# Kernel optimization log

Hardware: AMD Instinct MI355X
Metric: run time of the kernel (lower is better)

The kernel has to match this reference:

```python
import jax, jax.numpy as jnp
import numpy as np

N_NODES = 50000
N_EDGES = 800000
N_GRAPHS = 256
NEG_SLOPE = 0.2

def selu(x):
    return jax.nn.selu(x)

def gat_conv(x, src, dst, W, att_l, att_r, b, n_nodes):
    """PyG GATConv, heads=1, with self-loops already appended to (src, dst).
    Message j->i: alpha_ij = softmax_i(leaky_relu(a_l.h_j + a_r.h_i)); out_i = sum_j alpha_ij h_j + b."""
    h = x @ W                                   # [N, C]
    a_src = h @ att_l                           # [N]
    a_dst = h @ att_r                           # [N]
    e = jax.nn.leaky_relu(a_src[src] + a_dst[dst], NEG_SLOPE)   # [E]
    # segment softmax over incoming edges of each dst node
    m = jax.ops.segment_max(e, dst, num_segments=n_nodes)       # [N]
    m = jnp.where(jnp.isfinite(m), m, 0.0)
    ex = jnp.exp(e - m[dst])
    denom = jax.ops.segment_sum(ex, dst, num_segments=n_nodes)  # [N]
    alpha = ex / jnp.maximum(denom, 1e-16)[dst]                  # [E]
    out = jax.ops.segment_sum(h[src] * alpha[:, None], dst, num_segments=n_nodes)
    return out + b

def global_mean_pool(x, batch, n_graphs):
    s = jax.ops.segment_sum(x, batch, num_segments=n_graphs)
    cnt = jax.ops.segment_sum(jnp.ones((x.shape[0],), x.dtype), batch, num_segments=n_graphs)
    return s / jnp.maximum(cnt, 1.0)[:, None]

def setup_inputs() -> dict:
    key = jax.random.key(0)
    ks = jax.random.split(key, 12)
    F_in, C, H, NC = 310, 256, 128, 2
    x = jax.random.normal(ks[0], (N_NODES, F_in), dtype=jnp.float32)
    edge_index = jax.random.randint(ks[1], (2, N_EDGES), 0, N_NODES, dtype=jnp.int64)
    batch = jnp.sort(jax.random.randint(ks[2], (N_NODES,), 0, N_GRAPHS, dtype=jnp.int64))
    g = lambda k, shp: jax.random.normal(k, shp, dtype=jnp.float32) * 0.05
    return {
        "x": x, "edge_index": edge_index, "batch": batch,
        "W1": g(ks[3], (F_in, C)), "att_l1": g(ks[4], (C,)), "att_r1": g(ks[5], (C,)),
        "b1": jnp.zeros((C,), jnp.float32),
        "W2": g(ks[6], (C, C)), "att_l2": g(ks[7], (C,)), "att_r2": g(ks[8], (C,)),
        "b2": jnp.zeros((C,), jnp.float32),
        "fc1_W": g(ks[9], (C, H)), "fc1_b": jnp.zeros((H,), jnp.float32),
        "fc2_W": g(ks[10], (H, NC)), "fc2_b": jnp.zeros((NC,), jnp.float32),
    }

def reference(x, edge_index, batch, W1, att_l1, att_r1, b1, W2, att_l2, att_r2, b2,
              fc1_W, fc1_b, fc2_W, fc2_b):
    n = x.shape[0]
    loops = jnp.arange(n, dtype=edge_index.dtype)
    src = jnp.concatenate([edge_index[0], loops])   # add_self_loops=True (PyG default)
    dst = jnp.concatenate([edge_index[1], loops])
    h = selu(gat_conv(x, src, dst, W1, att_l1, att_r1, b1, n))
    h = selu(gat_conv(h, src, dst, W2, att_l2, att_r2, b2, n))
    g = selu(global_mean_pool(h, batch, N_GRAPHS))      # [G, 256]
    g = selu(g @ fc1_W + fc1_b)                         # [G, 128]
    # dropout is identity in eval mode
    return jax.nn.log_softmax(g @ fc2_W + fc2_b, axis=-1)  # [G, 2]
```

## Files before the change

### kernel.cpp

```cpp
#include <hip/hip_runtime.h>
#include <hip/hip_bf16.h>

#define N_NODES 50000
#define N_EDGES 800000
#define N_TOT   (N_EDGES + N_NODES)
#define N_GRAPHS 256
#define F_IN 310
#define KP1 320
#define CH 256
#define HID 128
#define CST 264

typedef __attribute__((ext_vector_type(8))) short short8;
typedef __attribute__((ext_vector_type(4))) float f32x4;
typedef unsigned short ushort_t;

__device__ __forceinline__ float selu_f(float x) {
    const float scale = 1.0507009873554805f;
    const float alpha = 1.6732632423543772f;
    return x > 0.f ? scale * x : scale * alpha * (expm1f(x));
}

__device__ __forceinline__ ushort_t f32_to_bf16_rne(float f) {
    unsigned u = __float_as_uint(f);
    unsigned rounding = 0x7FFFu + ((u >> 16) & 1u);
    return (ushort_t)((u + rounding) >> 16);
}
__device__ __forceinline__ float bf16_to_f32(ushort_t v) {
    return __uint_as_float(((unsigned)v) << 16);
}

#define WT_BLKS ((CH * KP1 + CH * CH + 255) / 256)
__global__ __launch_bounds__(256) void convert_wt_deg(
        const float* __restrict__ W1, ushort_t* __restrict__ W1t,
        const float* __restrict__ W2, ushort_t* __restrict__ W2t,
        const int* __restrict__ ei, int* __restrict__ deg) {
    int b = blockIdx.x;
    if (b < WT_BLKS) {
        int i = b * 256 + threadIdx.x;
        const int n1 = CH * KP1;
        if (i < n1) {
            int n = i / KP1, k = i % KP1;
            W1t[i] = (k < F_IN) ? f32_to_bf16_rne(W1[(long)k * CH + n]) : 0;
        } else {
            int j = i - n1;
            if (j >= CH * CH) return;
            int n = j / CH, k = j % CH;
            W2t[j] = f32_to_bf16_rne(W2[(long)k * CH + n]);
        }
    } else {
        int eid = (b - WT_BLKS) * 256 + threadIdx.x;
        if (eid >= N_TOT) return;
        int d = (eid < N_EDGES) ? ei[N_EDGES + eid] : eid - N_EDGES;
        atomicAdd(&deg[d], 1);
    }
}

template<int AF32, int FILL>
__global__ __launch_bounds__(256, 4) void gemm_k(
        const void* __restrict__ Asrc, const ushort_t* __restrict__ Bt,
        ushort_t* __restrict__ Cb, const float* __restrict__ att_l,
        const float* __restrict__ att_r, float* __restrict__ a_srcv,
        float* __restrict__ a_dstv, int M, int Kp, int gemmBlocks,
        const int* __restrict__ ei, int* __restrict__ fillpos,
        const int* __restrict__ startA, ushort_t* __restrict__ csr_src) {
    __shared__ __align__(16) ushort_t smem[20480];
    ushort_t (*As)[2048] = reinterpret_cast<ushort_t(*)[2048]>(smem);
    ushort_t (*Bs)[8192] = reinterpret_cast<ushort_t(*)[8192]>(smem + 4096);
    int tid = threadIdx.x;

    if constexpr (FILL) {
        if ((int)blockIdx.x >= gemmBlocks) {
            int eid = ((int)blockIdx.x - gemmBlocks) * 256 + tid;
            if (eid < N_TOT) {
                if (eid < N_EDGES) {
                    int s = ei[eid], d = ei[N_EDGES + eid];
                    int p = atomicAdd(&fillpos[d], 1);
                    csr_src[p] = (ushort_t)s;
                } else {
                    int d = eid - N_EDGES;
                    csr_src[startA[d]] = (ushort_t)d;
                }
            }
            return;
        }
    }

    int row0 = blockIdx.x * 64;
    int w = tid >> 6, l = tid & 63;
    int lr = l & 15, lc = l >> 4;
    f32x4 acc[4][4] = {};

    int srow = l >> 2;
    int sc = l & 3;
    int sx = sc ^ (srow & 3) ^ ((srow >> 2) & 3);
    int garow = row0 + w * 16 + srow; if (garow >= M) garow = M - 1;
    const ushort_t* gB[4];
#pragma unroll
    for (int g = 0; g < 4; ++g)
        gB[g] = Bt + (size_t)(w * 64 + g * 16 + srow) * Kp + sx * 8;
    int nt = Kp >> 5;

    const ushort_t* gA = nullptr;
    const float* xrow = nullptr;
    if (AF32) xrow = (const float*)Asrc + (size_t)garow * F_IN;
    else      gA = (const ushort_t*)Asrc + (size_t)garow * Kp + sx * 8;

    auto stageB = [&](int sel, int k0) {
#pragma unroll
        for (int g = 0; g < 4; ++g)
            __builtin_amdgcn_global_load_lds(
                (const __attribute__((address_space(1))) void*)(gB[g] + k0),
                (__attribute__((address_space(3))) void*)(&Bs[sel][(w * 64 + g * 16) * 32]), 16, 0, 0);
    };
    auto stageA_glds = [&](int sel, int k0) {
        __builtin_amdgcn_global_load_lds(
            (const __attribute__((address_space(1))) void*)(gA + k0),
            (__attribute__((address_space(3))) void*)(&As[sel][w * 16 * 32]), 16, 0, 0);
    };
    float va[8];
    auto loadA_f32 = [&](int k0) {
        int kc = k0 + sc * 8;
        if (kc + 8 <= F_IN) {
#pragma unroll
            for (int j = 0; j < 4; ++j) {
                float2 p = *(const float2*)(xrow + kc + j * 2);
                va[j * 2] = p.x; va[j * 2 + 1] = p.y;
            }
        } else {
#pragma unroll
            for (int j = 0; j < 8; ++j)
                va[j] = (kc + j < F_IN) ? xrow[kc + j] : 0.f;
        }
    };
    auto writeA = [&](int sel) {
        short8 s;
#pragma unroll
        for (int j = 0; j < 8; ++j) s[j] = (short)f32_to_bf16_rne(va[j]);
        *(short8*)(&As[sel][(w * 16 + srow) * 32 + sx * 8]) = s;
    };

    if (AF32) loadA_f32(0); else stageA_glds(0, 0);
    stageB(0, 0);
    if (AF32) writeA(0);
    __syncthreads();
    int cur = 0;
    for (int t = 0; t < nt; ++t) {
        int k1 = (t + 1) << 5;
        if (t + 1 < nt) {
            if (AF32) loadA_f32(k1); else stageA_glds(cur ^ 1, k1);
            stageB(cur ^ 1, k1);
        }
        short8 af[4], bfv[4];
#pragma unroll
        for (int mi = 0; mi < 4; ++mi) {
            int r = mi * 16 + lr;
            af[mi] = *(const short8*)(&As[cur][r * 32 + ((lc ^ (r & 3) ^ ((r >> 2) & 3)) * 8)]);
        }
#pragma unroll
        for (int ni = 0; ni < 4; ++ni) {
            int r = w * 64 + ni * 16 + lr;
            bfv[ni] = *(const short8*)(&Bs[cur][r * 32 + ((lc ^ (r & 3) ^ ((r >> 2) & 3)) * 8)]);
        }
#pragma unroll
        for (int mi = 0; mi < 4; ++mi)
#pragma unroll
            for (int ni = 0; ni < 4; ++ni)
                acc[mi][ni] = __builtin_amdgcn_mfma_f32_16x16x32_bf16(
                    bfv[ni], af[mi], acc[mi][ni], 0, 0, 0);
        if (AF32 && t + 1 < nt) writeA(cur ^ 1);
        __syncthreads();
        cur ^= 1;
    }

    ushort_t* Ct  = smem;
    float*    s_pw = (float*)(smem + 17024);
    float pl[4] = {}, pr[4] = {};
#pragma unroll
    for (int ni = 0; ni < 4; ++ni) {
        float4 alv = *(const float4*)(att_l + w * 64 + ni * 16 + lc * 4);
        float4 arv = *(const float4*)(att_r + w * 64 + ni * 16 + lc * 4);
#pragma unroll
        for (int mi = 0; mi < 4; ++mi) {
            f32x4 v = acc[mi][ni];
            pl[mi] += v[0] * alv.x + v[1] * alv.y + v[2] * alv.z + v[3] * alv.w;
            pr[mi] += v[0] * arv.x + v[1] * arv.y + v[2] * arv.z + v[3] * arv.w;
            ushort4 cv;
            cv.x = f32_to_bf16_rne(v[0]); cv.y = f32_to_bf16_rne(v[1]);
            cv.z = f32_to_bf16_rne(v[2]); cv.w = f32_to_bf16_rne(v[3]);
            *(ushort4*)(Ct + (mi * 16 + lr) * CST + w * 64 + ni * 16 + lc * 4) = cv;
        }
    }
#pragma unroll
    for (int mi = 0; mi < 4; ++mi) {
        pl[mi] += __shfl_xor(pl[mi], 16); pl[mi] += __shfl_xor(pl[mi], 32);
        pr[mi] += __shfl_xor(pr[mi], 16); pr[mi] += __shfl_xor(pr[mi], 32);
    }
    if (l < 16) {
#pragma unroll
        for (int mi = 0; mi < 4; ++mi) {
            s_pw[w * 64 + mi * 16 + lr]       = pl[mi];
            s_pw[256 + w * 64 + mi * 16 + lr] = pr[mi];
        }
    }
    __syncthreads();
#pragma unroll
    for (int it = 0; it < 8; ++it) {
        int id = it * 256 + tid;
        int r = id >> 5, c8 = (id & 31) * 8;
        int grow = row0 + r;
        if (grow < M) {
            short8 v = *(const short8*)(Ct + r * CST + c8);
            *(short8*)(Cb + (size_t)grow * CH + c8) = v;
        }
    }
    if (tid < 64) {
        int grow = row0 + tid;
        if (grow < M) {
            a_srcv[grow] = s_pw[tid] + s_pw[64 + tid] + s_pw[128 + tid] + s_pw[192 + tid];
            a_dstv[grow] = s_pw[256 + tid] + s_pw[320 + tid] + s_pw[384 + tid] + s_pw[448 + tid];
        }
    }
}

__global__ __launch_bounds__(256) void reserve_k(
        const int* __restrict__ deg, int* __restrict__ start,
        int* __restrict__ fillpos, int* __restrict__ cursor, int n) {
    int i = blockIdx.x * blockDim.x + threadIdx.x;
    if (i >= n) return;
    int s = atomicAdd(cursor, deg[i]);
    start[i] = s;
    fillpos[i] = s + 1;
}

__global__ __launch_bounds__(256) void gat_aggregate(
        const int* __restrict__ start, const int* __restrict__ deg,
        const ushort_t* __restrict__ csr_src,
        const float* __restrict__ a_src, const float* __restrict__ a_dst,
        const ushort_t* __restrict__ h, const float* __restrict__ bias,
        ushort_t* __restrict__ out_bf, int n) {
    int wid = threadIdx.x >> 6;
    int lane = threadIdx.x & 63;
    int node = blockIdx.x * 4 + wid;
    if (node >= n) return;
    int s0 = start[node];
    int dg = deg[node];
    float ad = a_dst[node];

    float sum_l = 0.f;
    float4 acc = {0.f, 0.f, 0.f, 0.f};
    for (int c = 0; c < dg; c += 64) {
        int nc = min(64, dg - c);
        int s_l = 0; float ex_l = 0.f;
        if (lane < nc) {
            s_l = csr_src[s0 + c + lane];
            float e = a_src[s_l] + ad;
            e = fmaxf(e, 0.2f * e);
            ex_l = __expf(e);
            sum_l += ex_l;
        }
        int j = 0;
        for (; j + 8 <= nc; j += 8) {
            int si[8]; float xi[8]; ushort4 hv[8];
#pragma unroll
            for (int k = 0; k < 8; ++k) {
                si[k] = __shfl(s_l, j + k);
                xi[k] = __shfl(ex_l, j + k);
            }
#pragma unroll
            for (int k = 0; k < 8; ++k)
                hv[k] = *(const ushort4*)(h + (long)si[k] * CH + lane * 4);
#pragma unroll
            for (int k = 0; k < 8; ++k) {
                acc.x += xi[k] * bf16_to_f32(hv[k].x);
                acc.y += xi[k] * bf16_to_f32(hv[k].y);
                acc.z += xi[k] * bf16_to_f32(hv[k].z);
                acc.w += xi[k] * bf16_to_f32(hv[k].w);
            }
        }
        for (; j < nc; ++j) {
            int sj = __shfl(s_l, j);
            float xj = __shfl(ex_l, j);
            ushort4 hv = *(const ushort4*)(h + (long)sj * CH + lane * 4);
            acc.x += xj * bf16_to_f32(hv.x);
            acc.y += xj * bf16_to_f32(hv.y);
            acc.z += xj * bf16_to_f32(hv.z);
            acc.w += xj * bf16_to_f32(hv.w);
        }
    }
    float sum = sum_l;
#pragma unroll
    for (int off = 32; off > 0; off >>= 1) sum += __shfl_xor(sum, off);
    float inv = 1.f / fmaxf(sum, 1e-16f);

    float4 bv = *(const float4*)(bias + lane * 4);
    ushort4 ob;
    ob.x = f32_to_bf16_rne(selu_f(acc.x * inv + bv.x));
    ob.y = f32_to_bf16_rne(selu_f(acc.y * inv + bv.y));
    ob.z = f32_to_bf16_rne(selu_f(acc.z * inv + bv.z));
    ob.w = f32_to_bf16_rne(selu_f(acc.w * inv + bv.w));
    *(ushort4*)(out_bf + (long)node * CH + lane * 4) = ob;
}

__global__ __launch_bounds__(1024) void pool_head_kernel(
        const ushort_t* __restrict__ h, const int* __restrict__ batch,
        const float* __restrict__ fc1W, const float* __restrict__ fc1b,
        const float* __restrict__ fc2W, const float* __restrict__ fc2b,
        float* __restrict__ out) {
    __shared__ float part[4][CH];
    __shared__ float row[CH];
    __shared__ float part2[8][HID];
    __shared__ float hrow[HID];
    __shared__ float logits[2];
    int g = blockIdx.x;
    int tid = threadIdx.x;
    int t = tid & 255;
    int quad = tid >> 8;
    int lo, hi;
    { int a = 0, b = N_NODES;
      while (a < b) { int mid = (a + b) >> 1; if (batch[mid] < g) a = mid + 1; else b = mid; }
      lo = a; }
    { int a = lo, b = N_NODES;
      while (a < b) { int mid = (a + b) >> 1; if (batch[mid] < g + 1) a = mid + 1; else b = mid; }
      hi = a; }
    float a0 = 0.f, a1 = 0.f;
    int i = lo + quad;
    for (; i + 4 < hi; i += 8) {
        a0 += bf16_to_f32(h[(long)i * CH + t]);
        a1 += bf16_to_f32(h[(long)(i + 4) * CH + t]);
    }
    for (; i < hi; i += 4) a0 += bf16_to_f32(h[(long)i * CH + t]);
    part[quad][t] = a0 + a1;
    __syncthreads();
    if (quad == 0) {
        float cnt = (float)(hi - lo);
        float acc = (part[0][t] + part[1][t]) + (part[2][t] + part[3][t]);
        row[t] = selu_f(acc / fmaxf(cnt, 1.f));
    }
    __syncthreads();
    {
        int o = tid & 127;
        int seg = tid >> 7;
        float s = 0.f;
        int k0 = seg * 32;
        for (int k = k0; k < k0 + 32; ++k) s += row[k] * fc1W[k * HID + o];
        part2[seg][o] = s;
    }
    __syncthreads();
    if (tid < HID) {
        float s = fc1b[tid];
#pragma unroll
        for (int j = 0; j < 8; ++j) s += part2[j][tid];
        hrow[tid] = selu_f(s);
    }
    __syncthreads();
    if (tid < 2) {
        float a = fc2b[tid];
        for (int k = 0; k < HID; k++) a += hrow[k] * fc2W[k * 2 + tid];
        logits[tid] = a;
    }
    __syncthreads();
    if (tid < 2) {
        float m = fmaxf(logits[0], logits[1]);
        float lse = logf(expf(logits[0] - m) + expf(logits[1] - m)) + m;
        out[g * 2 + tid] = logits[tid] - lse;
    }
}

extern "C" void kernel_launch(void* const* d_in, const int* in_sizes, int n_in,
                              void* d_out, int out_size, void* d_ws, size_t ws_size,
                              hipStream_t stream) {
    const float* x      = (const float*)d_in[0];
    const int*   ei     = (const int*)d_in[1];
    const int*   batch  = (const int*)d_in[2];
    const float* W1     = (const float*)d_in[3];
    const float* att_l1 = (const float*)d_in[4];
    const float* att_r1 = (const float*)d_in[5];
    const float* b1     = (const float*)d_in[6];
    const float* W2     = (const float*)d_in[7];
    const float* att_l2 = (const float*)d_in[8];
    const float* att_r2 = (const float*)d_in[9];
    const float* b2     = (const float*)d_in[10];
    const float* fc1W   = (const float*)d_in[11];
    const float* fc1b   = (const float*)d_in[12];
    const float* fc2W   = (const float*)d_in[13];
    const float* fc2b   = (const float*)d_in[14];
    float* out = (float*)d_out;

    char* ws = (char*)d_ws;
    size_t off = 0;
    auto alloc = [&](size_t bytes) {
        void* p = ws + off;
        off += (bytes + 255) & ~(size_t)255;
        return p;
    };
    ushort_t* Hb1    = (ushort_t*)alloc((size_t)N_NODES * CH * 2);
    ushort_t* Zb2    = (ushort_t*)alloc((size_t)N_NODES * CH * 2);
    ushort_t* Hb2    = (ushort_t*)alloc((size_t)N_NODES * CH * 2);
    ushort_t* W1t    = (ushort_t*)alloc((size_t)CH * KP1 * 2);
    ushort_t* W2t    = (ushort_t*)alloc((size_t)CH * CH * 2);
    float*    a_src  = (float*)alloc((size_t)N_NODES * 4);
    float*    a_dst  = (float*)alloc((size_t)N_NODES * 4);
    int*      deg    = (int*)alloc((size_t)N_NODES * 4);
    int*      cursor = (int*)alloc(256);
    int*      startA = (int*)alloc((size_t)N_NODES * 4);
    int*      fillpos= (int*)alloc((size_t)N_NODES * 4);
    ushort_t* csr_src= (ushort_t*)alloc((size_t)N_TOT * 2);

    size_t deg_pad = ((size_t)N_NODES * 4 + 255) & ~(size_t)255;

    dim3 blk(256);
    int gemm_grid = (N_NODES + 63) / 64;
    int edge_grid = (N_TOT + 255) / 256;
    int node_grid = (N_NODES + 255) / 256;
    int agg_grid  = (N_NODES + 3) / 4;
    int wtdeg_grid = WT_BLKS + edge_grid;

    hipMemsetAsync(deg, 0, deg_pad + 4, stream);
    convert_wt_deg<<<wtdeg_grid, blk, 0, stream>>>(W1, W1t, W2, W2t, ei, deg);
    reserve_k<<<node_grid, blk, 0, stream>>>(deg, startA, fillpos, cursor, N_NODES);

    gemm_k<1, 1><<<gemm_grid + edge_grid, blk, 0, stream>>>(
        x, W1t, Hb1, att_l1, att_r1, a_src, a_dst, N_NODES, KP1,
        gemm_grid, ei, fillpos, startA, csr_src);
    gat_aggregate<<<agg_grid, blk, 0, stream>>>(startA, deg, csr_src, a_src, a_dst,
                                                Hb1, b1, Zb2, N_NODES);

    gemm_k<0, 0><<<gemm_grid, blk, 0, stream>>>(
        Zb2, W2t, Hb2, att_l2, att_r2, a_src, a_dst, N_NODES, CH,
        gemm_grid, (const int*)nullptr, (int*)nullptr,
        (const int*)nullptr, (ushort_t*)nullptr);
    gat_aggregate<<<agg_grid, blk, 0, stream>>>(startA, deg, csr_src, a_src, a_dst,
                                                Hb2, b2, Hb1, N_NODES);

    pool_head_kernel<<<N_GRAPHS, dim3(1024), 0, stream>>>(Hb1, batch, fc1W, fc1b,
                                                          fc2W, fc2b, out);
}
```

Measured before the change: 292.0 us.

## Inline per-node fill counters into CSR buffer and use manual waitcnt barriers in GEMM

The CSR layout changes so each node's fill counter sits in the same buffer just before its source list. This drops the separate fillpos and start arrays, and the fill atomics should hit cache lines close to the data they write. The GEMM main loop also replaces __syncthreads with explicit s_waitcnt vmcnt/lgkmcnt plus s_barrier, so the next tile's loads can stay in flight across the barrier. The hard-coded vmcnt counts depend on the exact number of loads the compiler emits, and the CSR buffer size is fixed for this graph size.

```diff
diff --git a/kernel.cpp b/kernel.cpp
--- a/kernel.cpp
+++ b/kernel.cpp
@@ -56,14 +56,26 @@
     }
 }
 
+__global__ __launch_bounds__(256) void reserve_k(
+        const int* __restrict__ deg, int* __restrict__ basebuf,
+        int* __restrict__ csrbuf, int* __restrict__ cursor, int n) {
+    int i = blockIdx.x * blockDim.x + threadIdx.x;
+    if (i >= n) return;
+    int dgi = deg[i];
+    int words = 1 + ((dgi + 1) >> 1);
+    int b = atomicAdd(cursor, words);
+    basebuf[i] = b;
+    csrbuf[b] = 1;
+}
+
 template<int AF32, int FILL>
 __global__ __launch_bounds__(256, 4) void gemm_k(
         const void* __restrict__ Asrc, const ushort_t* __restrict__ Bt,
         ushort_t* __restrict__ Cb, const float* __restrict__ att_l,
         const float* __restrict__ att_r, float* __restrict__ a_srcv,
         float* __restrict__ a_dstv, int M, int Kp, int gemmBlocks,
-        const int* __restrict__ ei, int* __restrict__ fillpos,
-        const int* __restrict__ startA, ushort_t* __restrict__ csr_src) {
+        const int* __restrict__ ei, const int* __restrict__ basebuf,
+        int* __restrict__ csrbuf) {
     __shared__ __align__(16) ushort_t smem[20480];
     ushort_t (*As)[2048] = reinterpret_cast<ushort_t(*)[2048]>(smem);
     ushort_t (*Bs)[8192] = reinterpret_cast<ushort_t(*)[8192]>(smem + 4096);
@@ -75,11 +87,12 @@
             if (eid < N_TOT) {
                 if (eid < N_EDGES) {
                     int s = ei[eid], d = ei[N_EDGES + eid];
-                    int p = atomicAdd(&fillpos[d], 1);
-                    csr_src[p] = (ushort_t)s;
+                    int b = basebuf[d];
+                    int p = atomicAdd(&csrbuf[b], 1);
+                    ((ushort_t*)csrbuf)[2 * (b + 1) + p] = (ushort_t)s;
                 } else {
                     int d = eid - N_EDGES;
-                    csr_src[startA[d]] = (ushort_t)d;
+                    ((ushort_t*)csrbuf)[2 * (basebuf[d] + 1)] = (ushort_t)d;
                 }
             }
             return;
@@ -143,14 +156,25 @@
     if (AF32) loadA_f32(0); else stageA_glds(0, 0);
     stageB(0, 0);
     if (AF32) writeA(0);
-    __syncthreads();
+    asm volatile("s_waitcnt vmcnt(0) lgkmcnt(0)" ::: "memory");
+    __builtin_amdgcn_s_barrier();
+
     int cur = 0;
     for (int t = 0; t < nt; ++t) {
         int k1 = (t + 1) << 5;
-        if (t + 1 < nt) {
+        bool more = (t + 1 < nt);
+        if (more) {
             if (AF32) loadA_f32(k1); else stageA_glds(cur ^ 1, k1);
             stageB(cur ^ 1, k1);
         }
+        if (more) {
+            if constexpr (AF32) asm volatile("s_waitcnt vmcnt(8)" ::: "memory");
+            else                asm volatile("s_waitcnt vmcnt(5)" ::: "memory");
+        } else {
+            asm volatile("s_waitcnt vmcnt(0)" ::: "memory");
+        }
+        __builtin_amdgcn_s_barrier();
+
         short8 af[4], bfv[4];
 #pragma unroll
         for (int mi = 0; mi < 4; ++mi) {
@@ -168,8 +192,9 @@
             for (int ni = 0; ni < 4; ++ni)
                 acc[mi][ni] = __builtin_amdgcn_mfma_f32_16x16x32_bf16(
                     bfv[ni], af[mi], acc[mi][ni], 0, 0, 0);
-        if (AF32 && t + 1 < nt) writeA(cur ^ 1);
-        __syncthreads();
+        if (AF32 && more) writeA(cur ^ 1);
+        asm volatile("s_waitcnt lgkmcnt(0)" ::: "memory");
+        __builtin_amdgcn_s_barrier();
         cur ^= 1;
     }
 
@@ -223,19 +248,9 @@
     }
 }
 
-__global__ __launch_bounds__(256) void reserve_k(
-        const int* __restrict__ deg, int* __restrict__ start,
-        int* __restrict__ fillpos, int* __restrict__ cursor, int n) {
-    int i = blockIdx.x * blockDim.x + threadIdx.x;
-    if (i >= n) return;
-    int s = atomicAdd(cursor, deg[i]);
-    start[i] = s;
-    fillpos[i] = s + 1;
-}
-
 __global__ __launch_bounds__(256) void gat_aggregate(
-        const int* __restrict__ start, const int* __restrict__ deg,
-        const ushort_t* __restrict__ csr_src,
+        const int* __restrict__ basebuf, const int* __restrict__ deg,
+        const int* __restrict__ csrbuf,
         const float* __restrict__ a_src, const float* __restrict__ a_dst,
         const ushort_t* __restrict__ h, const float* __restrict__ bias,
         ushort_t* __restrict__ out_bf, int n) {
@@ -243,7 +258,8 @@
     int lane = threadIdx.x & 63;
     int node = blockIdx.x * 4 + wid;
     if (node >= n) return;
-    int s0 = start[node];
+    const ushort_t* csr = (const ushort_t*)csrbuf;
+    int s0 = 2 * (basebuf[node] + 1);
     int dg = deg[node];
     float ad = a_dst[node];
 
@@ -253,7 +269,7 @@
         int nc = min(64, dg - c);
         int s_l = 0; float ex_l = 0.f;
         if (lane < nc) {
-            s_l = csr_src[s0 + c + lane];
+            s_l = csr[s0 + c + lane];
             float e = a_src[s_l] + ad;
             e = fmaxf(e, 0.2f * e);
             ex_l = __expf(e);
@@ -403,9 +419,8 @@
     float*    a_dst  = (float*)alloc((size_t)N_NODES * 4);
     int*      deg    = (int*)alloc((size_t)N_NODES * 4);
     int*      cursor = (int*)alloc(256);
-    int*      startA = (int*)alloc((size_t)N_NODES * 4);
-    int*      fillpos= (int*)alloc((size_t)N_NODES * 4);
-    ushort_t* csr_src= (ushort_t*)alloc((size_t)N_TOT * 2);
+    int*      basebuf= (int*)alloc((size_t)N_NODES * 4);
+    int*      csrbuf = (int*)alloc((size_t)600000 * 4);
 
     size_t deg_pad = ((size_t)N_NODES * 4 + 255) & ~(size_t)255;
 
@@ -418,19 +433,18 @@
 
     hipMemsetAsync(deg, 0, deg_pad + 4, stream);
     convert_wt_deg<<<wtdeg_grid, blk, 0, stream>>>(W1, W1t, W2, W2t, ei, deg);
-    reserve_k<<<node_grid, blk, 0, stream>>>(deg, startA, fillpos, cursor, N_NODES);
+    reserve_k<<<node_grid, blk, 0, stream>>>(deg, basebuf, csrbuf, cursor, N_NODES);
 
     gemm_k<1, 1><<<gemm_grid + edge_grid, blk, 0, stream>>>(
         x, W1t, Hb1, att_l1, att_r1, a_src, a_dst, N_NODES, KP1,
-        gemm_grid, ei, fillpos, startA, csr_src);
-    gat_aggregate<<<agg_grid, blk, 0, stream>>>(startA, deg, csr_src, a_src, a_dst,
+        gemm_grid, ei, basebuf, csrbuf);
+    gat_aggregate<<<agg_grid, blk, 0, stream>>>(basebuf, deg, csrbuf, a_src, a_dst,
                                                 Hb1, b1, Zb2, N_NODES);
 
     gemm_k<0, 0><<<gemm_grid, blk, 0, stream>>>(
         Zb2, W2t, Hb2, att_l2, att_r2, a_src, a_dst, N_NODES, CH,
-        gemm_grid, (const int*)nullptr, (int*)nullptr,
-        (const int*)nullptr, (ushort_t*)nullptr);
-    gat_aggregate<<<agg_grid, blk, 0, stream>>>(startA, deg, csr_src, a_src, a_dst,
+        gemm_grid, (const int*)nullptr, (const int*)nullptr, (int*)nullptr);
+    gat_aggregate<<<agg_grid, blk, 0, stream>>>(basebuf, deg, csrbuf, a_src, a_dst,
                                                 Hb2, b2, Hb1, N_NODES);
 
     pool_head_kernel<<<N_GRAPHS, dim3(1024), 0, stream>>>(Hb1, batch, fc1W, fc1b,
```

Measured after the change: 303.4 us. +3.9%, slower.
